# Kernel tuning notes

Measured on AMD Instinct MI355X. Metric: run time of the kernel, lower is better.

The kernel has to match this reference:

```python
import jax, jax.numpy as jnp
import numpy as np

B, C, H, W = 8, 512, 64, 64
C8 = C // 8


def setup_inputs() -> dict:
    key = jax.random.key(0)
    ks = jax.random.split(key, 9)
    s = 1.0 / np.sqrt(C)
    return {
        "view1": jax.random.normal(ks[0], (B, C, H, W), jnp.float32),
        "view2": jax.random.normal(ks[1], (B, C, H, W), jnp.float32),
        "Wq": jax.random.normal(ks[2], (C8, C), jnp.float32) * s,
        "bq": jax.random.normal(ks[3], (C8,), jnp.float32) * 0.01,
        "Wk": jax.random.normal(ks[4], (C8, C), jnp.float32) * s,
        "bk": jax.random.normal(ks[5], (C8,), jnp.float32) * 0.01,
        "Wv": jax.random.normal(ks[6], (C, C), jnp.float32) * s,
        "bv": jax.random.normal(ks[7], (C,), jnp.float32) * 0.01,
        "gamma": jnp.array([0.5], jnp.float32),  # nn.Parameter(zeros(1)) in torch; nonzero here for nontrivial output
    }


def reference(view1, view2, Wq, bq, Wk, bk, Wv, bv, gamma):
    b, c, h, w = view1.shape
    n = h * w
    # 1x1 convs == per-pixel linear over channel dim
    q = jnp.einsum("bchw,oc->bohw", view1, Wq) + bq[None, :, None, None]
    k = jnp.einsum("bchw,oc->bohw", view2, Wk) + bk[None, :, None, None]
    v = jnp.einsum("bchw,oc->bohw", view2, Wv) + bv[None, :, None, None]
    q = q.reshape(b, -1, n).transpose(0, 2, 1)  # (B, N, C/8)
    k = k.reshape(b, -1, n)                      # (B, C/8, N)
    v = v.reshape(b, c, n)                       # (B, C, N)
    # no scaling, matching the original module
    attn = jax.nn.softmax(jnp.einsum("bnd,bdm->bnm", q, k), axis=-1)  # (B, N, N)
    out = jnp.einsum("bcn,bmn->bcm", v, attn).reshape(b, c, h, w)
    return gamma[0] * out + view1
```

## Files before the change

### kernel.cpp

```cpp
#include <hip/hip_runtime.h>

#define NB 8
#define NC 512
#define NPIX 4096
#define LOG2E 1.44269504088896340736f
#define C0TERM 28.853900817779268f

typedef __attribute__((ext_vector_type(4))) float f32x4;
typedef __attribute__((ext_vector_type(8))) short bf16x8;
typedef __attribute__((ext_vector_type(4))) unsigned short u16x4;

static __device__ __forceinline__ short f2bf(float f){
    union { float f; unsigned u; } v; v.f = f;
    unsigned r = v.u + 0x7fffu + ((v.u >> 16) & 1u);
    return (short)(r >> 16);
}

static __device__ __forceinline__ void gload16(const void* g, void* l){
    __builtin_amdgcn_global_load_lds(
        (const __attribute__((address_space(1))) char*)g,
        (__attribute__((address_space(3))) char*)l, 16, 0, 0);
}

__global__ void k_wconv(const float* __restrict__ wq, const float* __restrict__ wk,
                        const float* __restrict__ wv,
                        short* __restrict__ wqb, short* __restrict__ wkb,
                        short* __restrict__ wvb){
    int i = blockIdx.x * 256 + threadIdx.x;
    if (i < 64*NC){ wqb[i] = f2bf(wq[i]); wkb[i] = f2bf(wk[i]); }
    if (i < NC*NC){ wvb[i] = f2bf(wv[i]); }
}

__global__ __launch_bounds__(256) void k_projq(const float* __restrict__ X,
                                               const short* __restrict__ W,
                                               const float* __restrict__ bias,
                                               short* __restrict__ out){
    const int b = blockIdx.y;
    const int wv = threadIdx.x >> 6;
    const int lane = threadIdx.x & 63;
    const int g = lane >> 4, c16 = lane & 15;
    const int n0w = blockIdx.x * 64 + wv * 16;
    const float* Xb = X + (size_t)b * NC * NPIX;

    f32x4 acc[4];
#pragma unroll
    for (int f = 0; f < 4; ++f) acc[f] = (f32x4){0.f,0.f,0.f,0.f};

    for (int c0 = 0; c0 < NC; c0 += 32){
        bf16x8 a;
#pragma unroll
        for (int j = 0; j < 8; ++j)
            a[j] = f2bf(Xb[(size_t)(c0 + 8*g + j) * NPIX + n0w + c16]);
#pragma unroll
        for (int f = 0; f < 4; ++f){
            bf16x8 bfr = *(const bf16x8*)(W + (size_t)(f*16 + c16) * NC + c0 + 8*g);
            acc[f] = __builtin_amdgcn_mfma_f32_16x16x32_bf16(a, bfr, acc[f], 0, 0, 0);
        }
    }
#pragma unroll
    for (int f = 0; f < 4; ++f){
        int o = f*16 + c16;
        float bo = bias[o];
#pragma unroll
        for (int i = 0; i < 4; ++i)
            out[((size_t)b*NPIX + n0w + 4*g + i)*64 + o] = f2bf(acc[f][i] + bo);
    }
}

__global__ __launch_bounds__(256) void k_projkv(const float* __restrict__ X,
                                                const short* __restrict__ Wv_,
                                                const float* __restrict__ bv_,
                                                const short* __restrict__ Wk_,
                                                const float* __restrict__ bk_,
                                                short* __restrict__ vout,
                                                short* __restrict__ kout){
    const int b = blockIdx.y;
    const int wv = threadIdx.x >> 6;
    const int lane = threadIdx.x & 63;
    const int g = lane >> 4, c16 = lane & 15;
    const int n0w = blockIdx.x * 32 + (wv & 1) * 16;
    const int oh = wv >> 1;
    const int o0v = oh * 256;
    const int o0k = oh * 32;
    const float* Xb = X + (size_t)b * NC * NPIX;

    f32x4 accv[16], acck[2];
#pragma unroll
    for (int f = 0; f < 16; ++f) accv[f] = (f32x4){0.f,0.f,0.f,0.f};
#pragma unroll
    for (int f = 0; f < 2;  ++f) acck[f] = (f32x4){0.f,0.f,0.f,0.f};

    for (int c0 = 0; c0 < NC; c0 += 32){
        bf16x8 a;
#pragma unroll
        for (int j = 0; j < 8; ++j)
            a[j] = f2bf(Xb[(size_t)(c0 + 8*g + j) * NPIX + n0w + c16]);
#pragma unroll
        for (int f = 0; f < 16; ++f){
            bf16x8 bfr = *(const bf16x8*)(Wv_ + (size_t)(o0v + f*16 + c16) * NC + c0 + 8*g);
            accv[f] = __builtin_amdgcn_mfma_f32_16x16x32_bf16(a, bfr, accv[f], 0, 0, 0);
        }
#pragma unroll
        for (int f = 0; f < 2; ++f){
            bf16x8 bfr = *(const bf16x8*)(Wk_ + (size_t)(o0k + f*16 + c16) * NC + c0 + 8*g);
            acck[f] = __builtin_amdgcn_mfma_f32_16x16x32_bf16(a, bfr, acck[f], 0, 0, 0);
        }
    }
#pragma unroll
    for (int f = 0; f < 16; ++f){
        int o = o0v + f*16 + c16;
        float bo = bv_[o];
        u16x4 pk;
#pragma unroll
        for (int i = 0; i < 4; ++i) pk[i] = (unsigned short)f2bf(accv[f][i] + bo);
        *(u16x4*)(vout + ((size_t)b*NC + o)*NPIX + n0w + 4*g) = pk;
    }
#pragma unroll
    for (int f = 0; f < 2; ++f){
        int o = o0k + f*16 + c16;
        float bo = bk_[o];
#pragma unroll
        for (int i = 0; i < 4; ++i)
            kout[((size_t)b*NPIX + n0w + 4*g + i)*64 + o] = f2bf(acck[f][i] + bo);
    }
}

__global__ __launch_bounds__(256) void k_qk(const short* __restrict__ qb,
                                            const short* __restrict__ kb,
                                            short* __restrict__ P,
                                            float* __restrict__ Lpart,
                                            int b0){
    __shared__ __align__(16) short Pt[64*256];
    const int m0 = blockIdx.x * 64;
    const int n0 = blockIdx.y * 256;
    const int bz = blockIdx.z;
    const int b  = b0 + bz;
    const int wv = threadIdx.x >> 6;
    const int lane = threadIdx.x & 63;
    const int g = lane >> 4, c16 = lane & 15;
    const int nsub = wv * 64;

    bf16x8 qf[4][2];
#pragma unroll
    for (int mf = 0; mf < 4; ++mf)
#pragma unroll
        for (int kk = 0; kk < 2; ++kk)
            qf[mf][kk] = *(const bf16x8*)(qb + ((size_t)b*NPIX + m0 + mf*16 + c16)*64 + kk*32 + 8*g);

    float lsum[4] = {0.f,0.f,0.f,0.f};
    char* Ptb = (char*)Pt;

#pragma unroll
    for (int nf = 0; nf < 4; ++nf){
        bf16x8 kf0 = *(const bf16x8*)(kb + ((size_t)b*NPIX + n0 + nsub + nf*16 + c16)*64 + 8*g);
        bf16x8 kf1 = *(const bf16x8*)(kb + ((size_t)b*NPIX + n0 + nsub + nf*16 + c16)*64 + 32 + 8*g);
#pragma unroll
        for (int mf = 0; mf < 4; ++mf){
            f32x4 s = (f32x4){0.f,0.f,0.f,0.f};
            s = __builtin_amdgcn_mfma_f32_16x16x32_bf16(kf0, qf[mf][0], s, 0,0,0);
            s = __builtin_amdgcn_mfma_f32_16x16x32_bf16(kf1, qf[mf][1], s, 0,0,0);
            u16x4 pk;
#pragma unroll
            for (int i = 0; i < 4; ++i){
                float p = exp2f(fmaf(s[i], LOG2E, -C0TERM));
                lsum[mf] += p;
                pk[i] = (unsigned short)f2bf(p);
            }
            int m = mf*16 + c16;
            int ncol = nsub + nf*16 + 4*g;
            *(u16x4*)(Ptb + m*512 + ((2*ncol) ^ ((m&7)<<4))) = pk;
        }
    }
    __syncthreads();

    {
        char* Pgb = (char*)(P + ((size_t)bz*NPIX + m0)*NPIX + n0);
        const int chunk = threadIdx.x & 31;
        const int row8  = threadIdx.x >> 5;
#pragma unroll
        for (int p = 0; p < 8; ++p){
            int row = p*8 + row8;
            f32x4 v = *(const f32x4*)(Ptb + row*512 + ((chunk*16) ^ ((row&7)<<4)));
            *(f32x4*)(Pgb + (size_t)row*(NPIX*2) + chunk*16) = v;
        }
    }

#pragma unroll
    for (int mf = 0; mf < 4; ++mf){
        lsum[mf] += __shfl_xor(lsum[mf], 16);
        lsum[mf] += __shfl_xor(lsum[mf], 32);
    }
    if (lane < 16){
        size_t base = ((size_t)bz*64 + blockIdx.y*4 + wv)*NPIX + m0 + lane;
#pragma unroll
        for (int mf = 0; mf < 4; ++mf)
            Lpart[base + mf*16] = lsum[mf];
    }
}

__global__ __launch_bounds__(256) void k_lred(const float* __restrict__ Lpart,
                                              const float* __restrict__ gamma,
                                              float* __restrict__ scale){
    int idx = blockIdx.x * 256 + threadIdx.x;
    int bz = idx >> 12, m = idx & 4095;
    float s = 0.f;
    for (int sl = 0; sl < 64; ++sl)
        s += Lpart[((size_t)bz*64 + sl)*NPIX + m];
    scale[idx] = gamma[0] / s;
}

__global__ __launch_bounds__(256) void k_pv(const short* __restrict__ vb,
                                            const short* __restrict__ P,
                                            const float* __restrict__ scale,
                                            const float* __restrict__ view1,
                                            float* __restrict__ out,
                                            int b0){
    __shared__ __align__(16) short At[2][128*64];
    __shared__ __align__(16) short Bt[2][128*64];
    const int p  = blockIdx.x + 4*blockIdx.y;
    const int mt = (p & 7) | (((p >> 5) & 3) << 3);
    const int ct = (p >> 3) & 3;
    const int c0 = ct * 128;
    const int m0 = mt * 128;
    const int bz = blockIdx.z;
    const int b  = b0 + bz;
    const int wv = threadIdx.x >> 6;
    const int lane = threadIdx.x & 63;
    const int g = lane >> 4, c16 = lane & 15;
    const int wc = wv & 1, wm = wv >> 1;
    const int lrow = lane >> 3;
    const int srcg = (lane & 7) ^ lrow;
    const int swz  = (c16 & 7) << 4;

    const char* Vg = (const char*)(vb + ((size_t)b*NC + c0)*NPIX);
    const char* Pg = (const char*)(P + ((size_t)bz*NPIX + m0)*NPIX);

    f32x4 acc[4][4];
#pragma unroll
    for (int cf = 0; cf < 4; ++cf)
#pragma unroll
        for (int mf = 0; mf < 4; ++mf) acc[cf][mf] = (f32x4){0.f,0.f,0.f,0.f};

    auto stage = [&](int buf, int t){
        size_t nbyte = (size_t)t * 64 * 2;
#pragma unroll
        for (int j = 0; j < 4; ++j){
            int r0 = wv*32 + j*8;
            int row = r0 + lrow;
            gload16(Vg + (size_t)row*(NPIX*2) + nbyte + srcg*16, (char*)&At[buf][0] + r0*128);
            gload16(Pg + (size_t)row*(NPIX*2) + nbyte + srcg*16, (char*)&Bt[buf][0] + r0*128);
        }
    };

    stage(0, 0);
    __syncthreads();

    for (int t = 0; t < 64; ++t){
        int buf = t & 1;
        if (t < 63) stage(buf ^ 1, t + 1);
        const char* A  = (const char*)&At[buf][0];
        const char* Bp = (const char*)&Bt[buf][0];
#pragma unroll
        for (int kk = 0; kk < 2; ++kk){
            bf16x8 af[4], bfm[4];
#pragma unroll
            for (int f = 0; f < 4; ++f){
                af[f]  = *(const bf16x8*)(A  + (wc*64 + f*16 + c16)*128 + ((kk*64 + g*16) ^ swz));
                bfm[f] = *(const bf16x8*)(Bp + (wm*64 + f*16 + c16)*128 + ((kk*64 + g*16) ^ swz));
            }
#pragma unroll
            for (int cf = 0; cf < 4; ++cf)
#pragma unroll
                for (int mf = 0; mf < 4; ++mf)
                    acc[cf][mf] = __builtin_amdgcn_mfma_f32_16x16x32_bf16(af[cf], bfm[mf], acc[cf][mf], 0,0,0);
        }
        __syncthreads();
    }

    float sc[4];
#pragma unroll
    for (int mf = 0; mf < 4; ++mf)
        sc[mf] = scale[(size_t)bz*NPIX + m0 + wm*64 + mf*16 + c16];
#pragma unroll
    for (int cf = 0; cf < 4; ++cf){
#pragma unroll
        for (int mf = 0; mf < 4; ++mf){
            int m = m0 + wm*64 + mf*16 + c16;
#pragma unroll
            for (int i = 0; i < 4; ++i){
                int c = c0 + wc*64 + cf*16 + 4*g + i;
                size_t idx = ((size_t)b*NC + c)*NPIX + m;
                out[idx] = sc[mf]*acc[cf][mf][i] + view1[idx];
            }
        }
    }
}

__global__ __launch_bounds__(512, 2) void k_attn(const short* __restrict__ qb,
                                                 const short* __restrict__ kb,
                                                 const short* __restrict__ vb,
                                                 const float* __restrict__ view1,
                                                 const float* __restrict__ gamma,
                                                 float* __restrict__ out){
    __shared__ __align__(16) short P[2][64*64];
    __shared__ float Lred[128];

    const int bid = blockIdx.x;
    const int b  = bid & 7;
    const int m0 = (bid >> 3) * 64;
    const int wv = threadIdx.x >> 6;
    const int lane = threadIdx.x & 63;
    const int g = lane >> 4, c16 = lane & 15;
    const int msubA = (wv & 3) * 16;
    const int nhalf = wv >> 2;
    const int c0w = wv * 64;

    const short* qrow = qb + ((size_t)b*NPIX + m0 + msubA + c16)*64 + 8*g;
    bf16x8 qa0 = *(const bf16x8*)qrow;
    bf16x8 qa1 = *(const bf16x8*)(qrow + 32);

    const size_t kbase = (size_t)b * NPIX * 64;
    const int mrow = msubA + c16;
    const int swz = (mrow & 7) << 4;
    float Lacc = 0.f;

    f32x4 acc[4][4];
#pragma unroll
    for (int f = 0; f < 4; ++f)
#pragma unroll
        for (int cf = 0; cf < 4; ++cf) acc[f][cf] = (f32x4){0.f,0.f,0.f,0.f};

    char* Pb0 = (char*)&P[0][0];
    char* Pb1 = (char*)&P[1][0];

    bf16x8 vrA[8], vrB[8], krA[4], krB[4];

    auto loadK = [&](int t, bf16x8 (&kr)[4]){
        const short* kp = kb + kbase + (size_t)(t*64 + nhalf*32 + c16)*64 + 8*g;
        kr[0] = *(const bf16x8*)kp;
        kr[1] = *(const bf16x8*)(kp + 32);
        kr[2] = *(const bf16x8*)(kp + 16*64);
        kr[3] = *(const bf16x8*)(kp + 16*64 + 32);
    };
    auto loadV = [&](int t, bf16x8 (&vr)[8]){
#pragma unroll
        for (int h = 0; h < 2; ++h)
#pragma unroll
            for (int cf = 0; cf < 4; ++cf)
                vr[h*4+cf] = *(const bf16x8*)(vb + ((size_t)b*NC + c0w + cf*16 + c16)*NPIX
                                              + t*64 + h*32 + 8*g);
    };

    auto compA = [&](bf16x8 kA, bf16x8 kB, int fn, char* pb){
        f32x4 s = (f32x4){0.f,0.f,0.f,0.f};
        s = __builtin_amdgcn_mfma_f32_16x16x32_bf16(kA, qa0, s, 0,0,0);
        s = __builtin_amdgcn_mfma_f32_16x16x32_bf16(kB, qa1, s, 0,0,0);
        u16x4 pk;
#pragma unroll
        for (int i = 0; i < 4; ++i){
            float p = exp2f(fmaf(s[i], LOG2E, -C0TERM));
            Lacc += p;
            pk[i] = (unsigned short)f2bf(p);
        }
        int nrel0 = nhalf*32 + fn*16 + 4*g;
        *(u16x4*)(pb + mrow*128 + ((2*nrel0) ^ swz)) = pk;
    };

    auto phaseB = [&](const char* pc, const bf16x8 (&vr)[8]){
#pragma unroll
        for (int h = 0; h < 2; ++h){
            bf16x8 pa[4];
#pragma unroll
            for (int f = 0; f < 4; ++f){
                int row = f*16 + c16;
                pa[f] = *(const bf16x8*)(pc + row*128 + ((h*64 + g*16) ^ ((row&7)<<4)));
            }
#pragma unroll
            for (int cf = 0; cf < 4; ++cf)
#pragma unroll
                for (int f = 0; f < 4; ++f)
                    acc[f][cf] = __builtin_amdgcn_mfma_f32_16x16x32_bf16(pa[f], vr[h*4+cf], acc[f][cf], 0,0,0);
        }
    };

    auto iter = [&](int t, char* bufA, const char* bufB,
                    const bf16x8 (&vcur)[8], bf16x8 (&vnext)[8],
                    const bf16x8 (&kcur)[4], bf16x8 (&knext)[4]){
        loadV(t+1, vnext);
        loadK(t+2 < 64 ? t+2 : 63, knext);
        __builtin_amdgcn_s_setprio(1);
        phaseB(bufB, vcur);
        __builtin_amdgcn_s_setprio(0);
        compA(kcur[0], kcur[1], 0, bufA);
        compA(kcur[2], kcur[3], 1, bufA);
        asm volatile("s_waitcnt lgkmcnt(0)" ::: "memory");
        __builtin_amdgcn_s_barrier();
    };

    loadV(0, vrA);
    loadK(0, krA);
    loadK(1, krB);
    compA(krA[0], krA[1], 0, Pb0);
    compA(krA[2], krA[3], 1, Pb0);
    asm volatile("s_waitcnt lgkmcnt(0)" ::: "memory");
    __builtin_amdgcn_s_barrier();

    for (int t2 = 0; t2 < 31; ++t2){
        iter(2*t2,     Pb1, Pb0, vrA, vrB, krB, krA);
        iter(2*t2 + 1, Pb0, Pb1, vrB, vrA, krA, krB);
    }
    iter(62, Pb1, Pb0, vrA, vrB, krB, krA);
    __builtin_amdgcn_s_setprio(1);
    phaseB(Pb1, vrB);
    __builtin_amdgcn_s_setprio(0);

    Lacc += __shfl_xor(Lacc, 16);
    Lacc += __shfl_xor(Lacc, 32);
    if (lane < 16) Lred[nhalf*64 + msubA + lane] = Lacc;
    __syncthreads();

    float gm = gamma[0];
#pragma unroll
    for (int f = 0; f < 4; ++f){
        float sc[4];
#pragma unroll
        for (int i = 0; i < 4; ++i){
            int r = f*16 + 4*g + i;
            float Ls = Lred[r] + Lred[64 + r];
            sc[i] = gm / Ls;
        }
#pragma unroll
        for (int cf = 0; cf < 4; ++cf){
            int c = c0w + cf*16 + c16;
            size_t base = ((size_t)b*NC + c)*NPIX + m0 + f*16 + 4*g;
            f32x4 v1 = *(const f32x4*)(view1 + base);
            f32x4 r;
#pragma unroll
            for (int i = 0; i < 4; ++i) r[i] = sc[i]*acc[f][cf][i] + v1[i];
            *(f32x4*)(out + base) = r;
        }
    }
}

extern "C" void kernel_launch(void* const* d_in, const int* in_sizes, int n_in,
                              void* d_out, int out_size, void* d_ws, size_t ws_size,
                              hipStream_t stream){
    const float* view1 = (const float*)d_in[0];
    const float* view2 = (const float*)d_in[1];
    const float* Wq    = (const float*)d_in[2];
    const float* bq    = (const float*)d_in[3];
    const float* Wk    = (const float*)d_in[4];
    const float* bk    = (const float*)d_in[5];
    const float* Wv    = (const float*)d_in[6];
    const float* bv    = (const float*)d_in[7];
    const float* gamma = (const float*)d_in[8];
    float* out = (float*)d_out;

    char* ws = (char*)d_ws;
    short* qbuf = (short*)(ws);
    short* kbuf = (short*)(ws + (size_t)4*1024*1024);
    short* vbuf = (short*)(ws + (size_t)8*1024*1024);
    short* wqb  = (short*)(ws + (size_t)40*1024*1024);
    short* wkb  = (short*)(ws + (size_t)40*1024*1024 + 64*1024);
    short* wvb  = (short*)(ws + (size_t)40*1024*1024 + 128*1024);
    float* scl  = (float*)(ws + (size_t)41*1024*1024);
    float* Lpart= (float*)(ws + (size_t)42*1024*1024);
    short* Pbuf = (short*)(ws + (size_t)50*1024*1024);

    const size_t FIXED = (size_t)50*1024*1024;
    const size_t PPB   = (size_t)NPIX*NPIX*2;
    int avail = 0;
    if (ws_size > FIXED){
        size_t nn = (ws_size - FIXED) / PPB;
        avail = nn > 8 ? 8 : (int)nn;
    }
    int nbc = (avail >= 8) ? 8 : (avail >= 4) ? 4 : (avail >= 2) ? 2 : avail;

    hipLaunchKernelGGL(k_wconv, dim3(1024), dim3(256), 0, stream, Wq, Wk, Wv, wqb, wkb, wvb);
    hipLaunchKernelGGL(k_projq,  dim3(64, 8),  dim3(256), 0, stream, view1, wqb, bq, qbuf);
    hipLaunchKernelGGL(k_projkv, dim3(128, 8), dim3(256), 0, stream, view2, wvb, bv, wkb, bk, vbuf, kbuf);

    if (nbc >= 1){
        for (int b0 = 0; b0 < NB; b0 += nbc){
            int nb = (NB - b0 < nbc) ? (NB - b0) : nbc;
            hipLaunchKernelGGL(k_qk,   dim3(64, 16, nb), dim3(256), 0, stream, qbuf, kbuf, Pbuf, Lpart, b0);
            hipLaunchKernelGGL(k_lred, dim3(nb*16),      dim3(256), 0, stream, Lpart, gamma, scl);
            hipLaunchKernelGGL(k_pv,   dim3(4, 32, nb),  dim3(256), 0, stream, vbuf, Pbuf, scl, view1, out, b0);
        }
    } else {
        hipLaunchKernelGGL(k_attn, dim3(512), dim3(512), 0, stream, qbuf, kbuf, vbuf, view1, gamma, out);
    }
}
```

Baseline: 458.4 us.

## Transpose view2 to bf16 pixel-major and split K/V projection into tiled GEMMs

Adds a transpose kernel that converts view2 to bf16 in pixel-major layout, stored in the P buffer region. New k_projv and k_projk kernels then run register-tiled MFMA GEMMs that load contiguous 16-byte fragments. This replaces the fused k_projkv, which did strided scalar fp32 loads with per-element bf16 conversion. The cost is an extra kernel pass and a scratch write of the transposed input, and the fallback path still uses the old kernel.

```diff
diff --git a/kernel.cpp b/kernel.cpp
--- a/kernel.cpp
+++ b/kernel.cpp
@@ -64,6 +64,131 @@
 #pragma unroll
         for (int i = 0; i < 4; ++i)
             out[((size_t)b*NPIX + n0w + 4*g + i)*64 + o] = f2bf(acc[f][i] + bo);
+    }
+}
+
+__global__ __launch_bounds__(256) void k_trans(const float* __restrict__ X,
+                                               short* __restrict__ Xt){
+    __shared__ __align__(16) short T[64][72];
+    const int n0 = blockIdx.x * 64;
+    const int c0 = blockIdx.y * 64;
+    const int b  = blockIdx.z;
+    const int t  = threadIdx.x;
+    {
+        const int cl = t >> 2;
+        const int nq = (t & 3) * 16;
+        const float* src = X + ((size_t)b*NC + c0 + cl)*NPIX + n0 + nq;
+#pragma unroll
+        for (int q = 0; q < 4; ++q){
+            f32x4 v = *(const f32x4*)(src + q*4);
+#pragma unroll
+            for (int i = 0; i < 4; ++i)
+                T[nq + q*4 + i][cl] = f2bf(v[i]);
+        }
+    }
+    __syncthreads();
+    {
+        const int n  = t >> 2;
+        const int cs = (t & 3) * 16;
+        short* dst = Xt + ((size_t)b*NPIX + n0 + n)*NC + c0 + cs;
+        *(f32x4*)dst       = *(const f32x4*)&T[n][cs];
+        *(f32x4*)(dst + 8) = *(const f32x4*)&T[n][cs + 8];
+    }
+}
+
+__global__ __launch_bounds__(256) void k_projv(const short* __restrict__ Xt,
+                                               const short* __restrict__ W,
+                                               const float* __restrict__ bias,
+                                               short* __restrict__ vout){
+    const int o0 = blockIdx.x * 128;
+    const int n0 = blockIdx.y * 128;
+    const int b  = blockIdx.z;
+    const int wv = threadIdx.x >> 6;
+    const int lane = threadIdx.x & 63;
+    const int g = lane >> 4, c16 = lane & 15;
+    const int wo = wv & 1, wn = wv >> 1;
+
+    const short* Xb = Xt + ((size_t)b*NPIX + n0 + wn*64)*NC;
+    const short* Wb = W + (size_t)(o0 + wo*64)*NC;
+
+    f32x4 acc[4][4];
+#pragma unroll
+    for (int nf = 0; nf < 4; ++nf)
+#pragma unroll
+        for (int of = 0; of < 4; ++of) acc[nf][of] = (f32x4){0.f,0.f,0.f,0.f};
+
+    for (int c0 = 0; c0 < NC; c0 += 32){
+        bf16x8 af[4], bf_[4];
+#pragma unroll
+        for (int f = 0; f < 4; ++f){
+            af[f]  = *(const bf16x8*)(Xb + (size_t)(f*16 + c16)*NC + c0 + 8*g);
+            bf_[f] = *(const bf16x8*)(Wb + (size_t)(f*16 + c16)*NC + c0 + 8*g);
+        }
+#pragma unroll
+        for (int nf = 0; nf < 4; ++nf)
+#pragma unroll
+            for (int of = 0; of < 4; ++of)
+                acc[nf][of] = __builtin_amdgcn_mfma_f32_16x16x32_bf16(af[nf], bf_[of], acc[nf][of], 0,0,0);
+    }
+
+#pragma unroll
+    for (int of = 0; of < 4; ++of){
+        int o = o0 + wo*64 + of*16 + c16;
+        float bo = bias[o];
+#pragma unroll
+        for (int nf = 0; nf < 4; ++nf){
+            int n = n0 + wn*64 + nf*16 + 4*g;
+            u16x4 pk;
+#pragma unroll
+            for (int i = 0; i < 4; ++i) pk[i] = (unsigned short)f2bf(acc[nf][of][i] + bo);
+            *(u16x4*)(vout + ((size_t)b*NC + o)*NPIX + n) = pk;
+        }
+    }
+}
+
+__global__ __launch_bounds__(256) void k_projk(const short* __restrict__ Xt,
+                                               const short* __restrict__ W,
+                                               const float* __restrict__ bias,
+                                               short* __restrict__ kout){
+    const int n0 = blockIdx.x * 256;
+    const int b  = blockIdx.y;
+    const int wv = threadIdx.x >> 6;
+    const int lane = threadIdx.x & 63;
+    const int g = lane >> 4, c16 = lane & 15;
+
+    const short* Xb = Xt + ((size_t)b*NPIX + n0 + wv*64)*NC;
+
+    f32x4 acc[4][4];
+#pragma unroll
+    for (int of = 0; of < 4; ++of)
+#pragma unroll
+        for (int nf = 0; nf < 4; ++nf) acc[of][nf] = (f32x4){0.f,0.f,0.f,0.f};
+
+    for (int c0 = 0; c0 < NC; c0 += 32){
+        bf16x8 af[4], bf_[4];
+#pragma unroll
+        for (int f = 0; f < 4; ++f){
+            af[f]  = *(const bf16x8*)(W + (size_t)(f*16 + c16)*NC + c0 + 8*g);
+            bf_[f] = *(const bf16x8*)(Xb + (size_t)(f*16 + c16)*NC + c0 + 8*g);
+        }
+#pragma unroll
+        for (int of = 0; of < 4; ++of)
+#pragma unroll
+            for (int nf = 0; nf < 4; ++nf)
+                acc[of][nf] = __builtin_amdgcn_mfma_f32_16x16x32_bf16(af[of], bf_[nf], acc[of][nf], 0,0,0);
+    }
+
+#pragma unroll
+    for (int nf = 0; nf < 4; ++nf){
+        int n = n0 + wv*64 + nf*16 + c16;
+#pragma unroll
+        for (int of = 0; of < 4; ++of){
+            int o = of*16 + 4*g;
+            u16x4 pk;
+#pragma unroll
+            for (int i = 0; i < 4; ++i) pk[i] = (unsigned short)f2bf(acc[of][nf][i] + bias[o+i]);
+            *(u16x4*)(kout + ((size_t)b*NPIX + n)*64 + o) = pk;
+        }
     }
 }
 
@@ -466,6 +591,7 @@
     float* scl  = (float*)(ws + (size_t)41*1024*1024);
     float* Lpart= (float*)(ws + (size_t)42*1024*1024);
     short* Pbuf = (short*)(ws + (size_t)50*1024*1024);
+    short* X2t  = Pbuf;
 
     const size_t FIXED = (size_t)50*1024*1024;
     const size_t PPB   = (size_t)NPIX*NPIX*2;
@@ -478,9 +604,11 @@
 
     hipLaunchKernelGGL(k_wconv, dim3(1024), dim3(256), 0, stream, Wq, Wk, Wv, wqb, wkb, wvb);
     hipLaunchKernelGGL(k_projq,  dim3(64, 8),  dim3(256), 0, stream, view1, wqb, bq, qbuf);
-    hipLaunchKernelGGL(k_projkv, dim3(128, 8), dim3(256), 0, stream, view2, wvb, bv, wkb, bk, vbuf, kbuf);
 
     if (nbc >= 1){
+        hipLaunchKernelGGL(k_trans, dim3(64, 8, 8), dim3(256), 0, stream, view2, X2t);
+        hipLaunchKernelGGL(k_projv, dim3(4, 32, 8), dim3(256), 0, stream, X2t, wvb, bv, vbuf);
+        hipLaunchKernelGGL(k_projk, dim3(16, 8),    dim3(256), 0, stream, X2t, wkb, bk, kbuf);
         for (int b0 = 0; b0 < NB; b0 += nbc){
             int nb = (NB - b0 < nbc) ? (NB - b0) : nbc;
             hipLaunchKernelGGL(k_qk,   dim3(64, 16, nb), dim3(256), 0, stream, qbuf, kbuf, Pbuf, Lpart, b0);
@@ -488,6 +616,7 @@
             hipLaunchKernelGGL(k_pv,   dim3(4, 32, nb),  dim3(256), 0, stream, vbuf, Pbuf, scl, view1, out, b0);
         }
     } else {
+        hipLaunchKernelGGL(k_projkv, dim3(128, 8), dim3(256), 0, stream, view2, wvb, bv, wkb, bk, vbuf, kbuf);
         hipLaunchKernelGGL(k_attn, dim3(512), dim3(512), 0, stream, qbuf, kbuf, vbuf, view1, gamma, out);
     }
 }
```

After: 413.0 us. -9.9%, faster.
